# Optimization experiments

Hardware: AMD Instinct MI355X
Metric: run time of the kernel (lower is better)

## Reference

```python
import jax, jax.numpy as jnp
import numpy as np

BN_EPS = 1e-5


def setup_inputs() -> dict:
    key = jax.random.key(0)
    ks = jax.random.split(key, 8)
    b, c, h, w, d = 16, 256, 128, 128, 64
    x = jax.random.normal(ks[0], (b, c, h, w), dtype=jnp.float32)
    conv1_w = jax.random.normal(ks[1], (c, c), dtype=jnp.float32) * np.sqrt(2.0 / c)
    conv1_b = jax.random.normal(ks[2], (c,), dtype=jnp.float32) * 0.02
    mk_w = jax.random.normal(ks[3], (d, c), dtype=jnp.float32) * np.sqrt(2.0 / d)
    mv_w = jnp.transpose(mk_w)  # original ties mv.weight = mk.weight.permute(1,0,2)
    conv2_w = jax.random.normal(ks[4], (c, c), dtype=jnp.float32) * np.sqrt(2.0 / c)
    bn_gamma = jnp.ones((c,), dtype=jnp.float32)
    bn_beta = jnp.zeros((c,), dtype=jnp.float32)
    bn_mean = jax.random.normal(ks[5], (c,), dtype=jnp.float32) * 0.1
    bn_var = jax.random.uniform(ks[6], (c,), dtype=jnp.float32, minval=0.5, maxval=1.5)
    return {"x": x, "conv1_w": conv1_w, "conv1_b": conv1_b, "mk_w": mk_w,
            "mv_w": mv_w, "conv2_w": conv2_w, "bn_gamma": bn_gamma,
            "bn_beta": bn_beta, "bn_mean": bn_mean, "bn_var": bn_var}


def reference(x, conv1_w, conv1_b, mk_w, mv_w, conv2_w, bn_gamma, bn_beta, bn_mean, bn_var):
    b, c, h, w = x.shape
    n = h * w
    identity = x
    # conv1: 1x1 conv with bias -> [b, c, n]
    y = jnp.einsum('oc,bchw->bohw', conv1_w, x) + conv1_b[None, :, None, None]
    y = y.reshape(b, c, n)
    # external attention: mk projection [b, d, n]
    attn = jnp.einsum('dc,bcn->bdn', mk_w, y)
    attn = jax.nn.softmax(attn, axis=-1)              # softmax over spatial N
    attn = attn / (1e-9 + attn.sum(axis=1, keepdims=True))  # column-normalize over d
    # mv projection back to channels [b, c, n]
    z = jnp.einsum('cd,bdn->bcn', mv_w, attn)
    z = z.reshape(b, c, h, w)
    # conv2 (1x1, no bias) + BatchNorm (inference) + residual + relu
    z = jnp.einsum('oc,bchw->bohw', conv2_w, z)
    inv = bn_gamma / jnp.sqrt(bn_var + BN_EPS)
    z = z * inv[None, :, None, None] + (bn_beta - bn_mean * inv)[None, :, None, None]
    return jax.nn.relu(z + identity)
```

## Files before the change

kernel.cpp:

```cpp
#include <hip/hip_runtime.h>
#include <hip/hip_bf16.h>

#define HW 16384
#define C  256
#define D  64
#define NB 16
#define M0 16.0f
#define LOG2E 1.44269504088896340736f

typedef unsigned short u16;
typedef __attribute__((ext_vector_type(4))) float  f32x4;
typedef __attribute__((ext_vector_type(4))) short  s16x4;
typedef __attribute__((ext_vector_type(8))) short  s16x8;

__device__ __forceinline__ float bf2f(u16 u) {
    return __uint_as_float(((unsigned int)u) << 16);
}
__device__ __forceinline__ short f2bfs(float f) {
    union { __hip_bfloat16 h; short s; } u;
    u.h = __float2bfloat16(f);
    return u.s;
}
__device__ __forceinline__ u16 f2bf(float f) {
    unsigned int u = __float_as_uint(f);
    unsigned int r = (u + 0x7fffu + ((u >> 16) & 1u)) >> 16;
    return (u16)r;
}

#define MFMA16(a, b, c) __builtin_amdgcn_mfma_f32_16x16x32_bf16((a), (b), (c), 0, 0, 0)

__global__ void precompute_kernel(const float* __restrict__ conv1_w,
                                  const float* __restrict__ conv1_b,
                                  const float* __restrict__ mk_w,
                                  const float* __restrict__ mv_w,
                                  const float* __restrict__ conv2_w,
                                  const float* __restrict__ gamma,
                                  const float* __restrict__ beta,
                                  const float* __restrict__ mean,
                                  const float* __restrict__ var,
                                  short* __restrict__ Ath,
                                  short* __restrict__ Atl,
                                  float* __restrict__ amk,
                                  short* __restrict__ Bmb,
                                  float* __restrict__ shift,
                                  float* __restrict__ esum)
{
    int gid = blockIdx.x * blockDim.x + threadIdx.x;
    if (gid < C * D) {
        int d = gid >> 8, cp = gid & 255;
        float s = 0.f;
        for (int c = 0; c < C; ++c) s += mk_w[d * C + c] * conv1_w[c * C + cp];
        u16 h = f2bf(s);
        Ath[gid] = (short)h;
        Atl[gid] = (short)f2bf(s - bf2f(h));
    } else if (gid < 2 * C * D) {
        int g = gid - C * D;
        int o = g >> 6, d = g & 63;
        float inv = gamma[o] * rsqrtf(var[o] + 1e-5f);
        float s = 0.f;
        for (int c = 0; c < C; ++c) s += conv2_w[o * C + c] * mv_w[c * D + d];
        Bmb[g] = (short)f2bf(s * inv);
    } else if (gid < 2 * C * D + D) {
        int d = gid - 2 * C * D;
        float s = 0.f;
        for (int c = 0; c < C; ++c) s += mk_w[d * C + c] * conv1_b[c];
        amk[d] = s;
    } else if (gid < 2 * C * D + D + C) {
        int o = gid - (2 * C * D + D);
        float inv = gamma[o] * rsqrtf(var[o] + 1e-5f);
        shift[o] = beta[o] - mean[o] * inv;
    } else if (gid < 2 * C * D + D + C + NB * D) {
        esum[gid - (2 * C * D + D + C)] = 0.f;
    }
}

#define NT1 64
#define XR  (C + 8)
__global__ __launch_bounds__(256, 3) void esum_kernel(const float* __restrict__ x,
                                                      const short* __restrict__ Ath,
                                                      const short* __restrict__ Atl,
                                                      const float* __restrict__ amk,
                                                      float* __restrict__ esum)
{
    __shared__ short xs[NT1 * XR];
    const int t = threadIdx.x;
    const int b = blockIdx.y;
    const int n0 = blockIdx.x * NT1;
    const int lane = t & 63, w = t >> 6;
    const int col = lane & 15, g = lane >> 4;

    const float* xb = x + (size_t)b * C * HW + n0;
    #pragma unroll
    for (int i = 0; i < 4; ++i) {
        int cell = i * 256 + t;
        int nq = cell & 15, cq = cell >> 4;
        int c0 = cq * 4, nn = nq * 4;
        const float* gp = xb + (size_t)c0 * HW + nn;
        f32x4 r0 = *(const f32x4*)(gp);
        f32x4 r1 = *(const f32x4*)(gp + HW);
        f32x4 r2 = *(const f32x4*)(gp + 2 * HW);
        f32x4 r3 = *(const f32x4*)(gp + 3 * HW);
        #pragma unroll
        for (int j = 0; j < 4; ++j) {
            s16x4 hi = { f2bfs(r0[j]), f2bfs(r1[j]), f2bfs(r2[j]), f2bfs(r3[j]) };
            *(s16x4*)&xs[(nn + j) * XR + c0] = hi;
        }
    }
    __syncthreads();

    s16x8 Ah[8], Al[8];
    {
        const short* ah = Ath + (size_t)(w * 16 + col) * C + 8 * g;
        const short* al = Atl + (size_t)(w * 16 + col) * C + 8 * g;
        #pragma unroll
        for (int ks = 0; ks < 8; ++ks) {
            Ah[ks] = *(const s16x8*)(ah + ks * 32);
            Al[ks] = *(const s16x8*)(al + ks * 32);
        }
    }

    f32x4 zz = {0.f, 0.f, 0.f, 0.f};
    f32x4 acc[4] = { zz, zz, zz, zz };
    #pragma unroll
    for (int ks = 0; ks < 8; ++ks) {
        #pragma unroll
        for (int nt = 0; nt < 4; ++nt) {
            s16x8 xf = *(const s16x8*)&xs[(nt * 16 + col) * XR + ks * 32 + 8 * g];
            acc[nt] = MFMA16(xf, Ah[ks], acc[nt]);
            acc[nt] = MFMA16(xf, Al[ks], acc[nt]);
        }
    }

    const float am = amk[w * 16 + col];
    float rs = 0.f;
    #pragma unroll
    for (int nt = 0; nt < 4; ++nt)
        #pragma unroll
        for (int r = 0; r < 4; ++r)
            rs += exp2f((acc[nt][r] + am - M0) * LOG2E);
    rs += __shfl_xor(rs, 16);
    rs += __shfl_xor(rs, 32);
    if (lane < 16) atomicAdd(esum + b * D + w * 16 + lane, rs);
}

#define NT3 64
__global__ __launch_bounds__(256, 3) void out_kernel(const float* __restrict__ x,
                                                     const short* __restrict__ Ath,
                                                     const short* __restrict__ Atl,
                                                     const float* __restrict__ amk,
                                                     const float* __restrict__ esum,
                                                     const short* __restrict__ Bmb,
                                                     const float* __restrict__ shift,
                                                     float* __restrict__ out)
{
    __shared__ short xs[NT3 * XR];
    __shared__ short ps[NT3 * 72];
    __shared__ float csum[4][NT3];
    __shared__ float rr[NT3];

    const int t = threadIdx.x;
    const int b  = (NB - 1) - blockIdx.y;
    const int n0 = ((int)gridDim.x - 1 - blockIdx.x) * NT3;
    const int lane = t & 63, w = t >> 6;
    const int col = lane & 15, g = lane >> 4;

    const float* xb = x + (size_t)b * C * HW + n0;
    #pragma unroll
    for (int i = 0; i < 4; ++i) {
        int cell = i * 256 + t;
        int nq = cell & 15, cq = cell >> 4;
        int c0 = cq * 4, nn = nq * 4;
        const float* gp = xb + (size_t)c0 * HW + nn;
        f32x4 r0 = *(const f32x4*)(gp);
        f32x4 r1 = *(const f32x4*)(gp + HW);
        f32x4 r2 = *(const f32x4*)(gp + 2 * HW);
        f32x4 r3 = *(const f32x4*)(gp + 3 * HW);
        #pragma unroll
        for (int j = 0; j < 4; ++j) {
            s16x4 hi = { f2bfs(r0[j]), f2bfs(r1[j]), f2bfs(r2[j]), f2bfs(r3[j]) };
            *(s16x4*)&xs[(nn + j) * XR + c0] = hi;
        }
    }
    __syncthreads();

    {
        s16x8 Ah[8], Al[8];
        const short* ah = Ath + (size_t)(w * 16 + col) * C + 8 * g;
        const short* al = Atl + (size_t)(w * 16 + col) * C + 8 * g;
        #pragma unroll
        for (int ks = 0; ks < 8; ++ks) {
            Ah[ks] = *(const s16x8*)(ah + ks * 32);
            Al[ks] = *(const s16x8*)(al + ks * 32);
        }

        f32x4 zz = {0.f, 0.f, 0.f, 0.f};
        f32x4 acc[4] = { zz, zz, zz, zz };
        #pragma unroll
        for (int ks = 0; ks < 8; ++ks) {
            #pragma unroll
            for (int nt = 0; nt < 4; ++nt) {
                s16x8 xf = *(const s16x8*)&xs[(nt * 16 + col) * XR + ks * 32 + 8 * g];
                acc[nt] = MFMA16(xf, Ah[ks], acc[nt]);
                acc[nt] = MFMA16(xf, Al[ks], acc[nt]);
            }
        }

        const float am  = amk[w * 16 + col];
        const float inv = __fdividef(1.0f, esum[b * D + w * 16 + col]);
        #pragma unroll
        for (int nt = 0; nt < 4; ++nt)
            #pragma unroll
            for (int r = 0; r < 4; ++r) {
                float e = exp2f((acc[nt][r] + am - M0) * LOG2E);
                ps[(nt * 16 + 4 * g + r) * 72 + w * 16 + col] = f2bfs(e * inv);
            }
    }
    __syncthreads();

    {
        const int nl = t & 63, dq = t >> 6;
        const short* pr = &ps[nl * 72 + dq * 16];
        s16x8 a0 = *(const s16x8*)(pr);
        s16x8 a1 = *(const s16x8*)(pr + 8);
        float cs = 0.f;
        #pragma unroll
        for (int k = 0; k < 8; ++k) cs += bf2f((u16)a0[k]) + bf2f((u16)a1[k]);
        csum[dq][nl] = cs;
    }
    __syncthreads();
    if (t < NT3)
        rr[t] = __fdividef(1.0f, csum[0][t] + csum[1][t] + csum[2][t] + csum[3][t] + 1e-9f);
    __syncthreads();

    s16x8 Bf[4][2];
    #pragma unroll
    for (int ot = 0; ot < 4; ++ot) {
        const short* bp = Bmb + (size_t)(w * 64 + ot * 16 + col) * D + 8 * g;
        Bf[ot][0] = *(const s16x8*)(bp);
        Bf[ot][1] = *(const s16x8*)(bp + 32);
    }

    f32x4 zz = {0.f, 0.f, 0.f, 0.f};
    f32x4 acc[4][4];
    #pragma unroll
    for (int ot = 0; ot < 4; ++ot)
        #pragma unroll
        for (int nt = 0; nt < 4; ++nt) acc[ot][nt] = zz;

    #pragma unroll
    for (int nt = 0; nt < 4; ++nt) {
        const short* pr = &ps[(nt * 16 + col) * 72 + 8 * g];
        s16x8 p0 = *(const s16x8*)(pr);
        s16x8 p1 = *(const s16x8*)(pr + 32);
        #pragma unroll
        for (int ot = 0; ot < 4; ++ot) {
            acc[ot][nt] = MFMA16(p0, Bf[ot][0], acc[ot][nt]);
            acc[ot][nt] = MFMA16(p1, Bf[ot][1], acc[ot][nt]);
        }
    }

    float sh[4];
    #pragma unroll
    for (int ot = 0; ot < 4; ++ot) sh[ot] = shift[w * 64 + ot * 16 + col];

    float* ob = out + (size_t)b * C * HW + n0;
    #pragma unroll
    for (int nt = 0; nt < 4; ++nt) {
        f32x4 rv = *(const f32x4*)&rr[nt * 16 + 4 * g];
        #pragma unroll
        for (int ot = 0; ot < 4; ++ot) {
            const size_t off = (size_t)(w * 64 + ot * 16 + col) * HW + nt * 16 + 4 * g;
            f32x4 xv = *(const f32x4*)(xb + off);
            f32x4 vv;
            #pragma unroll
            for (int r = 0; r < 4; ++r)
                vv[r] = fmaxf(acc[ot][nt][r] * rv[r] + sh[ot] + xv[r], 0.f);
            __builtin_nontemporal_store(vv, (f32x4*)(ob + off));
        }
    }
}

extern "C" void kernel_launch(void* const* d_in, const int* in_sizes, int n_in,
                              void* d_out, int out_size, void* d_ws, size_t ws_size,
                              hipStream_t stream)
{
    const float* x       = (const float*)d_in[0];
    const float* conv1_w = (const float*)d_in[1];
    const float* conv1_b = (const float*)d_in[2];
    const float* mk_w    = (const float*)d_in[3];
    const float* mv_w    = (const float*)d_in[4];
    const float* conv2_w = (const float*)d_in[5];
    const float* gamma   = (const float*)d_in[6];
    const float* beta    = (const float*)d_in[7];
    const float* mean    = (const float*)d_in[8];
    const float* var     = (const float*)d_in[9];
    float* out = (float*)d_out;

    float* amk   = (float*)d_ws;
    float* shift = amk + D;
    float* esum  = shift + C;
    short* Ath   = (short*)(esum + NB * D);
    short* Atl   = Ath + C * D;
    short* Bmb   = Atl + C * D;

    const int pre_work = 2 * C * D + D + C + NB * D;
    precompute_kernel<<<(pre_work + 255) / 256, 256, 0, stream>>>(
        conv1_w, conv1_b, mk_w, mv_w, conv2_w, gamma, beta, mean, var,
        Ath, Atl, amk, Bmb, shift, esum);

    esum_kernel<<<dim3(HW / NT1, NB), 256, 0, stream>>>(x, Ath, Atl, amk, esum);

    out_kernel<<<dim3(HW / NT3, NB), 256, 0, stream>>>(x, Ath, Atl, amk, esum,
                                                       Bmb, shift, out);
}
```

Baseline: 578.6 us.

## Split channel staging into halves and chunk output GEMM to raise occupancy

Both kernels now stage the input tile in two 128-channel halves through a smaller shared buffer, holding only half of the A fragments in registers at a time. The output kernel also computes the conv2 projection in two 128-channel passes with fewer accumulators. Launch bounds rise from 3 to 5 and 4 blocks per CU. The aim is to cut LDS and register pressure so more waves can hide memory latency. The cost is extra barriers and less load-level parallelism per block.

Result: faster. 566.9 us (-2.0%).

```diff
diff --git a/kernel.cpp b/kernel.cpp
--- a/kernel.cpp
+++ b/kernel.cpp
@@ -75,14 +75,15 @@
 }
 
 #define NT1 64
-#define XR  (C + 8)
-__global__ __launch_bounds__(256, 3) void esum_kernel(const float* __restrict__ x,
+#define CH  128
+#define XR1 (CH + 8)
+__global__ __launch_bounds__(256, 5) void esum_kernel(const float* __restrict__ x,
                                                       const short* __restrict__ Ath,
                                                       const short* __restrict__ Atl,
                                                       const float* __restrict__ amk,
                                                       float* __restrict__ esum)
 {
-    __shared__ short xs[NT1 * XR];
+    __shared__ short xs[NT1 * XR1];
     const int t = threadIdx.x;
     const int b = blockIdx.y;
     const int n0 = blockIdx.x * NT1;
@@ -90,44 +91,51 @@
     const int col = lane & 15, g = lane >> 4;
 
     const float* xb = x + (size_t)b * C * HW + n0;
-    #pragma unroll
-    for (int i = 0; i < 4; ++i) {
-        int cell = i * 256 + t;
-        int nq = cell & 15, cq = cell >> 4;
-        int c0 = cq * 4, nn = nq * 4;
-        const float* gp = xb + (size_t)c0 * HW + nn;
-        f32x4 r0 = *(const f32x4*)(gp);
-        f32x4 r1 = *(const f32x4*)(gp + HW);
-        f32x4 r2 = *(const f32x4*)(gp + 2 * HW);
-        f32x4 r3 = *(const f32x4*)(gp + 3 * HW);
-        #pragma unroll
-        for (int j = 0; j < 4; ++j) {
-            s16x4 hi = { f2bfs(r0[j]), f2bfs(r1[j]), f2bfs(r2[j]), f2bfs(r3[j]) };
-            *(s16x4*)&xs[(nn + j) * XR + c0] = hi;
-        }
-    }
-    __syncthreads();
-
-    s16x8 Ah[8], Al[8];
-    {
-        const short* ah = Ath + (size_t)(w * 16 + col) * C + 8 * g;
-        const short* al = Atl + (size_t)(w * 16 + col) * C + 8 * g;
-        #pragma unroll
-        for (int ks = 0; ks < 8; ++ks) {
-            Ah[ks] = *(const s16x8*)(ah + ks * 32);
-            Al[ks] = *(const s16x8*)(al + ks * 32);
-        }
-    }
 
     f32x4 zz = {0.f, 0.f, 0.f, 0.f};
     f32x4 acc[4] = { zz, zz, zz, zz };
-    #pragma unroll
-    for (int ks = 0; ks < 8; ++ks) {
-        #pragma unroll
-        for (int nt = 0; nt < 4; ++nt) {
-            s16x8 xf = *(const s16x8*)&xs[(nt * 16 + col) * XR + ks * 32 + 8 * g];
-            acc[nt] = MFMA16(xf, Ah[ks], acc[nt]);
-            acc[nt] = MFMA16(xf, Al[ks], acc[nt]);
+
+    for (int h = 0; h < 2; ++h) {
+        const int ch = h * CH;
+        if (h) __syncthreads();
+
+        #pragma unroll
+        for (int i = 0; i < 2; ++i) {
+            int cell = i * 256 + t;
+            int nq = cell & 15, cq = cell >> 4;
+            int c0 = cq * 4, nn = nq * 4;
+            const float* gp = xb + (size_t)(ch + c0) * HW + nn;
+            f32x4 r0 = *(const f32x4*)(gp);
+            f32x4 r1 = *(const f32x4*)(gp + HW);
+            f32x4 r2 = *(const f32x4*)(gp + 2 * HW);
+            f32x4 r3 = *(const f32x4*)(gp + 3 * HW);
+            #pragma unroll
+            for (int j = 0; j < 4; ++j) {
+                s16x4 hi = { f2bfs(r0[j]), f2bfs(r1[j]), f2bfs(r2[j]), f2bfs(r3[j]) };
+                *(s16x4*)&xs[(nn + j) * XR1 + c0] = hi;
+            }
+        }
+
+        s16x8 Ah[4], Al[4];
+        {
+            const short* ah = Ath + (size_t)(w * 16 + col) * C + ch + 8 * g;
+            const short* al = Atl + (size_t)(w * 16 + col) * C + ch + 8 * g;
+            #pragma unroll
+            for (int ks = 0; ks < 4; ++ks) {
+                Ah[ks] = *(const s16x8*)(ah + ks * 32);
+                Al[ks] = *(const s16x8*)(al + ks * 32);
+            }
+        }
+        __syncthreads();
+
+        #pragma unroll
+        for (int ks = 0; ks < 4; ++ks) {
+            #pragma unroll
+            for (int nt = 0; nt < 4; ++nt) {
+                s16x8 xf = *(const s16x8*)&xs[(nt * 16 + col) * XR1 + ks * 32 + 8 * g];
+                acc[nt] = MFMA16(xf, Ah[ks], acc[nt]);
+                acc[nt] = MFMA16(xf, Al[ks], acc[nt]);
+            }
         }
     }
 
@@ -143,8 +151,8 @@
     if (lane < 16) atomicAdd(esum + b * D + w * 16 + lane, rs);
 }
 
-#define NT3 64
-__global__ __launch_bounds__(256, 3) void out_kernel(const float* __restrict__ x,
+#define PR3 72
+__global__ __launch_bounds__(256, 4) void out_kernel(const float* __restrict__ x,
                                                      const short* __restrict__ Ath,
                                                      const short* __restrict__ Atl,
                                                      const float* __restrict__ amk,
@@ -153,73 +161,83 @@
                                                      const float* __restrict__ shift,
                                                      float* __restrict__ out)
 {
-    __shared__ short xs[NT3 * XR];
-    __shared__ short ps[NT3 * 72];
-    __shared__ float csum[4][NT3];
-    __shared__ float rr[NT3];
+    __shared__ short xs[NT1 * XR1];
+    __shared__ short ps[NT1 * PR3];
+    __shared__ float csum[4][NT1];
+    __shared__ float rr[NT1];
 
     const int t = threadIdx.x;
     const int b  = (NB - 1) - blockIdx.y;
-    const int n0 = ((int)gridDim.x - 1 - blockIdx.x) * NT3;
+    const int n0 = ((int)gridDim.x - 1 - blockIdx.x) * NT1;
     const int lane = t & 63, w = t >> 6;
     const int col = lane & 15, g = lane >> 4;
 
     const float* xb = x + (size_t)b * C * HW + n0;
-    #pragma unroll
-    for (int i = 0; i < 4; ++i) {
-        int cell = i * 256 + t;
-        int nq = cell & 15, cq = cell >> 4;
-        int c0 = cq * 4, nn = nq * 4;
-        const float* gp = xb + (size_t)c0 * HW + nn;
-        f32x4 r0 = *(const f32x4*)(gp);
-        f32x4 r1 = *(const f32x4*)(gp + HW);
-        f32x4 r2 = *(const f32x4*)(gp + 2 * HW);
-        f32x4 r3 = *(const f32x4*)(gp + 3 * HW);
-        #pragma unroll
-        for (int j = 0; j < 4; ++j) {
-            s16x4 hi = { f2bfs(r0[j]), f2bfs(r1[j]), f2bfs(r2[j]), f2bfs(r3[j]) };
-            *(s16x4*)&xs[(nn + j) * XR + c0] = hi;
-        }
-    }
-    __syncthreads();
 
     {
-        s16x8 Ah[8], Al[8];
-        const short* ah = Ath + (size_t)(w * 16 + col) * C + 8 * g;
-        const short* al = Atl + (size_t)(w * 16 + col) * C + 8 * g;
-        #pragma unroll
-        for (int ks = 0; ks < 8; ++ks) {
-            Ah[ks] = *(const s16x8*)(ah + ks * 32);
-            Al[ks] = *(const s16x8*)(al + ks * 32);
-        }
-
         f32x4 zz = {0.f, 0.f, 0.f, 0.f};
         f32x4 acc[4] = { zz, zz, zz, zz };
-        #pragma unroll
-        for (int ks = 0; ks < 8; ++ks) {
-            #pragma unroll
-            for (int nt = 0; nt < 4; ++nt) {
-                s16x8 xf = *(const s16x8*)&xs[(nt * 16 + col) * XR + ks * 32 + 8 * g];
-                acc[nt] = MFMA16(xf, Ah[ks], acc[nt]);
-                acc[nt] = MFMA16(xf, Al[ks], acc[nt]);
+
+        for (int h = 0; h < 2; ++h) {
+            const int ch = h * CH;
+            if (h) __syncthreads();
+
+            #pragma unroll
+            for (int i = 0; i < 2; ++i) {
+                int cell = i * 256 + t;
+                int nq = cell & 15, cq = cell >> 4;
+                int c0 = cq * 4, nn = nq * 4;
+                const float* gp = xb + (size_t)(ch + c0) * HW + nn;
+                f32x4 r0 = *(const f32x4*)(gp);
+                f32x4 r1 = *(const f32x4*)(gp + HW);
+                f32x4 r2 = *(const f32x4*)(gp + 2 * HW);
+                f32x4 r3 = *(const f32x4*)(gp + 3 * HW);
+                #pragma unroll
+                for (int j = 0; j < 4; ++j) {
+                    s16x4 hi = { f2bfs(r0[j]), f2bfs(r1[j]), f2bfs(r2[j]), f2bfs(r3[j]) };
+                    *(s16x4*)&xs[(nn + j) * XR1 + c0] = hi;
+                }
+            }
+
+            s16x8 Ah[4], Al[4];
+            {
+                const short* ah = Ath + (size_t)(w * 16 + col) * C + ch + 8 * g;
+                const short* al = Atl + (size_t)(w * 16 + col) * C + ch + 8 * g;
+                #pragma unroll
+                for (int ks = 0; ks < 4; ++ks) {
+                    Ah[ks] = *(const s16x8*)(ah + ks * 32);
+                    Al[ks] = *(const s16x8*)(al + ks * 32);
+                }
+            }
+            __syncthreads();
+
+            #pragma unroll
+            for (int ks = 0; ks < 4; ++ks) {
+                #pragma unroll
+                for (int nt = 0; nt < 4; ++nt) {
+                    s16x8 xf = *(const s16x8*)&xs[(nt * 16 + col) * XR1 + ks * 32 + 8 * g];
+                    acc[nt] = MFMA16(xf, Ah[ks], acc[nt]);
+                    acc[nt] = MFMA16(xf, Al[ks], acc[nt]);
+                }
             }
         }
 
         const float am  = amk[w * 16 + col];
         const float inv = __fdividef(1.0f, esum[b * D + w * 16 + col]);
+        __syncthreads();
         #pragma unroll
         for (int nt = 0; nt < 4; ++nt)
             #pragma unroll
             for (int r = 0; r < 4; ++r) {
                 float e = exp2f((acc[nt][r] + am - M0) * LOG2E);
-                ps[(nt * 16 + 4 * g + r) * 72 + w * 16 + col] = f2bfs(e * inv);
+                ps[(nt * 16 + 4 * g + r) * PR3 + w * 16 + col] = f2bfs(e * inv);
             }
     }
     __syncthreads();
 
     {
         const int nl = t & 63, dq = t >> 6;
-        const short* pr = &ps[nl * 72 + dq * 16];
+        const short* pr = &ps[nl * PR3 + dq * 16];
         s16x8 a0 = *(const s16x8*)(pr);
         s16x8 a1 = *(const s16x8*)(pr + 8);
         float cs = 0.f;
@@ -228,54 +246,58 @@
         csum[dq][nl] = cs;
     }
     __syncthreads();
-    if (t < NT3)
+    if (t < NT1)
         rr[t] = __fdividef(1.0f, csum[0][t] + csum[1][t] + csum[2][t] + csum[3][t] + 1e-9f);
     __syncthreads();
 
-    s16x8 Bf[4][2];
-    #pragma unroll
-    for (int ot = 0; ot < 4; ++ot) {
-        const short* bp = Bmb + (size_t)(w * 64 + ot * 16 + col) * D + 8 * g;
-        Bf[ot][0] = *(const s16x8*)(bp);
-        Bf[ot][1] = *(const s16x8*)(bp + 32);
-    }
-
-    f32x4 zz = {0.f, 0.f, 0.f, 0.f};
-    f32x4 acc[4][4];
-    #pragma unroll
-    for (int ot = 0; ot < 4; ++ot)
-        #pragma unroll
-        for (int nt = 0; nt < 4; ++nt) acc[ot][nt] = zz;
-
-    #pragma unroll
-    for (int nt = 0; nt < 4; ++nt) {
-        const short* pr = &ps[(nt * 16 + col) * 72 + 8 * g];
-        s16x8 p0 = *(const s16x8*)(pr);
-        s16x8 p1 = *(const s16x8*)(pr + 32);
-        #pragma unroll
-        for (int ot = 0; ot < 4; ++ot) {
-            acc[ot][nt] = MFMA16(p0, Bf[ot][0], acc[ot][nt]);
-            acc[ot][nt] = MFMA16(p1, Bf[ot][1], acc[ot][nt]);
-        }
-    }
-
-    float sh[4];
-    #pragma unroll
-    for (int ot = 0; ot < 4; ++ot) sh[ot] = shift[w * 64 + ot * 16 + col];
-
     float* ob = out + (size_t)b * C * HW + n0;
-    #pragma unroll
-    for (int nt = 0; nt < 4; ++nt) {
-        f32x4 rv = *(const f32x4*)&rr[nt * 16 + 4 * g];
-        #pragma unroll
-        for (int ot = 0; ot < 4; ++ot) {
-            const size_t off = (size_t)(w * 64 + ot * 16 + col) * HW + nt * 16 + 4 * g;
-            f32x4 xv = *(const f32x4*)(xb + off);
-            f32x4 vv;
-            #pragma unroll
-            for (int r = 0; r < 4; ++r)
-                vv[r] = fmaxf(acc[ot][nt][r] * rv[r] + sh[ot] + xv[r], 0.f);
-            __builtin_nontemporal_store(vv, (f32x4*)(ob + off));
+    for (int oh = 0; oh < 2; ++oh) {
+        const int ob0 = oh * 128 + w * 32;
+
+        s16x8 Bf[2][2];
+        #pragma unroll
+        for (int ot = 0; ot < 2; ++ot) {
+            const short* bp = Bmb + (size_t)(ob0 + ot * 16 + col) * D + 8 * g;
+            Bf[ot][0] = *(const s16x8*)(bp);
+            Bf[ot][1] = *(const s16x8*)(bp + 32);
+        }
+
+        f32x4 zz = {0.f, 0.f, 0.f, 0.f};
+        f32x4 acc2[2][4];
+        #pragma unroll
+        for (int ot = 0; ot < 2; ++ot)
+            #pragma unroll
+            for (int nt = 0; nt < 4; ++nt) acc2[ot][nt] = zz;
+
+        #pragma unroll
+        for (int nt = 0; nt < 4; ++nt) {
+            const short* pr = &ps[(nt * 16 + col) * PR3 + 8 * g];
+            s16x8 p0 = *(const s16x8*)(pr);
+            s16x8 p1 = *(const s16x8*)(pr + 32);
+            #pragma unroll
+            for (int ot = 0; ot < 2; ++ot) {
+                acc2[ot][nt] = MFMA16(p0, Bf[ot][0], acc2[ot][nt]);
+                acc2[ot][nt] = MFMA16(p1, Bf[ot][1], acc2[ot][nt]);
+            }
+        }
+
+        float sh[2];
+        #pragma unroll
+        for (int ot = 0; ot < 2; ++ot) sh[ot] = shift[ob0 + ot * 16 + col];
+
+        #pragma unroll
+        for (int nt = 0; nt < 4; ++nt) {
+            f32x4 rv = *(const f32x4*)&rr[nt * 16 + 4 * g];
+            #pragma unroll
+            for (int ot = 0; ot < 2; ++ot) {
+                const size_t off = (size_t)(ob0 + ot * 16 + col) * HW + nt * 16 + 4 * g;
+                f32x4 xv = *(const f32x4*)(xb + off);
+                f32x4 vv;
+                #pragma unroll
+                for (int r = 0; r < 4; ++r)
+                    vv[r] = fmaxf(acc2[ot][nt][r] * rv[r] + sh[ot] + xv[r], 0.f);
+                __builtin_nontemporal_store(vv, (f32x4*)(ob + off));
+            }
         }
     }
 }
@@ -310,6 +332,6 @@
 
     esum_kernel<<<dim3(HW / NT1, NB), 256, 0, stream>>>(x, Ath, Atl, amk, esum);
 
-    out_kernel<<<dim3(HW / NT3, NB), 256, 0, stream>>>(x, Ath, Atl, amk, esum,
+    out_kernel<<<dim3(HW / NT1, NB), 256, 0, stream>>>(x, Ath, Atl, amk, esum,
                                                        Bmb, shift, out);
 }
```
